# Kernel optimization log

Measured on AMD Instinct MI355X. Metric: run time of the kernel, lower is better.

The kernel has to match this reference:

```python
import jax, jax.numpy as jnp
import numpy as np
from math import factorial

# ---- architecture constants (from S2ConvNet_original.__init__) ----
B_IN, B_L1, B_L2 = 30, 15, 10
F1, F2, NCLS = 20, 40, 10
BATCH = 32

# ---------- numpy precompute: Wigner small-d matrices and quadrature ----------

def wigner_d(l, beta):
    """Wigner small-d matrix d^l_{m,n}(beta) for all m,n, vectorized over beta.
    Returns [len(beta), 2l+1, 2l+1] with centered indices (row m+l, col n+l)."""
    beta = np.atleast_1d(np.asarray(beta, dtype=np.float64))
    cb, sb = np.cos(beta / 2), np.sin(beta / 2)
    d = np.zeros((beta.size, 2 * l + 1, 2 * l + 1))
    for m in range(-l, l + 1):
        for n in range(-l, l + 1):
            pref = np.sqrt(float(factorial(l + m) * factorial(l - m) * factorial(l + n) * factorial(l - n)))
            s = np.zeros_like(beta)
            for k in range(max(0, m - n), min(l + m, l - n) + 1):
                c = (-1.0) ** k / float(factorial(k) * factorial(l + m - k) * factorial(l - n - k) * factorial(n - m + k))
                s += c * cb ** (2 * l + m - n - 2 * k) * sb ** (n - m + 2 * k)
            d[:, m + l, n + l] = pref * s
    return d

def wigner_stack(nl, betas):
    """Zero-padded stack of d^l matrices: [nl, n_beta, 2nl-1, 2nl-1], centered at nl-1."""
    M, c = 2 * nl - 1, nl - 1
    D = np.zeros((nl, len(betas), M, M))
    for l in range(nl):
        D[l, :, c - l:c + l + 1, c - l:c + l + 1] = wigner_d(l, betas)
    return D

def dh_weights(b):
    """Driscoll-Healy / SOFT quadrature weights over the 2b beta samples."""
    j = np.arange(2 * b); k = np.arange(b)
    s = (np.sin(np.outer(2 * j + 1, 2 * k + 1) * np.pi / (4 * b)) / (2 * k + 1)).sum(axis=1)
    return (2.0 / b) * np.sin(np.pi * (2 * j + 1) / (4 * b)) * s

def soft_betas(b):
    return np.pi * (2 * np.arange(2 * b) + 1) / (4 * b)

def centered_freqs(nl, n):
    # map centered m in [-(nl-1), nl-1] to fft bin indices of length-n transform
    return (np.arange(2 * nl - 1) - (nl - 1)) % n

# ---- conv1 (S2 -> SO3), b_in=30, b_out=15 ----
NL1, M1 = B_L1, 2 * B_L1 - 1
_D1F = wigner_stack(NL1, soft_betas(B_IN))[:, :, :, NL1 - 1] * dh_weights(B_IN)[None, :, None]  # [15,60,29]
_D1I = wigner_stack(NL1, soft_betas(B_L1))  # [15,30,29,29]
FQI1 = centered_freqs(NL1, 2 * B_IN)
FQO1 = centered_freqs(NL1, 2 * B_L1)
# s2_near_identity_grid: max_beta=pi/8, n_alpha=8, n_beta=3 -> 24 points
_gb = np.arange(1, 4) * (np.pi / 8) / 3
_ga = np.linspace(0, 2 * np.pi, 8, endpoint=False)
GB1, GA1 = [g.ravel() for g in np.meshgrid(_gb, _ga, indexing='ij')]
_m1 = np.arange(M1) - (NL1 - 1)
_Y1 = ((2 * np.arange(NL1) + 1.0)[:, None, None]
       * wigner_stack(NL1, GB1)[:, :, :, NL1 - 1].transpose(0, 2, 1)
       * np.exp(-1j * np.outer(_m1, GA1))[None])  # [15,29,24] spherical-harmonic basis at grid

# ---- conv2 (SO3 -> SO3), b_in=15, b_out=10 ----
NL2, M2 = B_L2, 2 * B_L2 - 1
_D2F = wigner_stack(NL2, soft_betas(B_L1)) * dh_weights(B_L1)[None, :, None, None]  # [10,30,19,19]
_D2I = wigner_stack(NL2, soft_betas(B_L2))  # [10,20,19,19]
FQI2 = centered_freqs(NL2, 2 * B_L1)
FQO2 = centered_freqs(NL2, 2 * B_L2)
# so3_near_identity_grid: 3 betas x 8 alphas x 8 gammas = 192 points
_gg = np.linspace(0, 2 * np.pi, 8, endpoint=False)
GB2, GA2, GG2 = [g.ravel() for g in np.meshgrid(_gb, _ga, _gg, indexing='ij')]
_m2 = np.arange(M2) - (NL2 - 1)
_Y2 = ((2 * np.arange(NL2) + 1.0)[:, None, None, None]
       * wigner_stack(NL2, GB2).transpose(0, 2, 3, 1)
       * np.exp(-1j * (np.outer(_m2, GA2)[:, None, :] + np.outer(_m2, GG2)[None, :, :]))[None])  # [10,19,19,192]

D1F = jnp.asarray(_D1F, jnp.float32); D1I = jnp.asarray(_D1I, jnp.float32); Y1 = jnp.asarray(_Y1, jnp.complex64)
D2F = jnp.asarray(_D2F, jnp.float32); D2I = jnp.asarray(_D2I, jnp.float32); Y2 = jnp.asarray(_Y2, jnp.complex64)
W_INT = jnp.asarray(dh_weights(B_L2), jnp.float32)  # [20]


def s2_conv(x, w, bias):
    # x: [B,1,60,60] (beta, alpha) -> SO3 signal [B,F1,30,30,30]
    xf = jnp.fft.fft(x, axis=-1)[..., FQI1]                       # [B,1,60,29] alpha-FFT, centered m
    X = jnp.einsum('bfjm,ljm->bflm', xf, D1F)                      # S2 FT: [B,1,15,29]
    psi = jnp.einsum('iog,lmg->lmio', w, Y1)                       # kernel S2 FT: [15,29,1,20]
    Z = jnp.einsum('bilm,lnio->bolmn', X, jnp.conj(psi))           # outer product m x n: [B,20,15,29,29]
    Fb = jnp.einsum('bolmn,ljmn->bojmn', Z, D1I)                   # beta synthesis: [B,20,30,29,29]
    n = 2 * B_L1
    full = jnp.zeros(Fb.shape[:3] + (n, n), Fb.dtype).at[..., FQO1[:, None], FQO1[None, :]].set(Fb)
    y = jnp.fft.ifft2(full, axes=(-2, -1)).real * (n * n)          # inverse alpha/gamma FFT
    return y + bias


def so3_conv(x, w, bias):
    # x: [B,F1,30,30,30] (beta, alpha, gamma) -> [B,F2,20,20,20]
    xf = jnp.fft.fft2(x, axes=(-2, -1))[..., FQI2[:, None], FQI2[None, :]]  # [B,20,30,19,19]
    X = jnp.einsum('bfjmn,ljmn->bflmn', xf, D2F)                   # SO3 FT: [B,20,10,19,19]
    psi = jnp.einsum('iog,lmng->lmnio', w, Y2)                     # kernel SO3 FT: [10,19,19,20,40]
    Z = jnp.einsum('bilmn,lknio->bolmk', X, jnp.conj(psi))         # Z^l = X^l @ Psi^l^H: [B,40,10,19,19]
    Fb = jnp.einsum('bolmk,ljmk->bojmk', Z, D2I)                   # [B,40,20,19,19]
    n = 2 * B_L2
    full = jnp.zeros(Fb.shape[:3] + (n, n), Fb.dtype).at[..., FQO2[:, None], FQO2[None, :]].set(Fb)
    y = jnp.fft.ifft2(full, axes=(-2, -1)).real * (n * n)
    return y + bias


def setup_inputs() -> dict:
    key = jax.random.key(0)
    ks = jax.random.split(key, 6)
    x = jax.random.normal(ks[0], (BATCH, 1, 2 * B_IN, 2 * B_IN), jnp.float32)
    w1 = jax.random.normal(ks[1], (1, F1, GB1.size), jnp.float32) / np.sqrt(GB1.size)
    b1 = jax.random.normal(ks[2], (1, F1, 1, 1, 1), jnp.float32) * 0.01
    w2 = jax.random.normal(ks[3], (F1, F2, GB2.size), jnp.float32) / np.sqrt(F1 * GB2.size)
    b2 = jax.random.normal(ks[4], (1, F2, 1, 1, 1), jnp.float32) * 0.01
    w_lin = jax.random.normal(ks[5], (NCLS, F2), jnp.float32) / np.sqrt(F2)
    bl_lin = jnp.zeros((NCLS,), jnp.float32)
    return {"x": x, "w1": w1, "b1": b1, "w2": w2, "b2": b2, "w_lin": w_lin, "bl_lin": bl_lin}


def reference(x, w1, b1, w2, b2, w_lin, bl_lin):
    h = jax.nn.relu(s2_conv(x, w1, b1))                            # [B,20,30,30,30]
    h = jax.nn.relu(so3_conv(h, w2, b2))                           # [B,40,20,20,20]
    # so3_integrate: quadrature over beta, uniform sums over alpha/gamma
    g = jnp.einsum('bfjkl,j->bf', h, W_INT) * (2 * np.pi / (2 * B_L2)) ** 2
    return g @ w_lin.T + bl_lin                                    # [B,10]
```

## Files before the change

kernel.cpp:

```cpp
#include <hip/hip_runtime.h>
#include <cmath>
#include <cstdio>

#ifndef M_PI
#define M_PI 3.14159265358979323846
#endif

#define OFF_D1F   0
#define OFF_D1IP  26100
#define OFF_D2FP  227940
#define OFF_D2IP  282090
#define OFF_Y1    318190
#define OFF_WI    339070
#define OFF_E1    339090
#define OFF_I1    342570
#define OFF_E2    344310
#define OFF_I2    345450
#define OFF_DHW30 346210
#define OFF_DHW15 346270
#define NCONST    346300

#define WOFF_CONST 0ul
#define WOFF_Y2BF  2457600ul
#define WOFF_W2BF  5406720ul
#define WOFF_AAUG  5750784ul
#define WOFF_BT    15581184ul
#define WOFF_H1    39174144ul
#define WOFF_CPSI  39174144ul
#define WOFF_Z     39174144ul
#define WOFF_H2    2457600ul
#define WOFF_XF1   76140544ul
#define WOFF_X1    (76140544ul + 445440ul)
#define WOFF_PSI1  (76140544ul + 445440ul + 111360ul)
#define WOFF_G     (76140544ul + 445440ul + 111360ul + 69600ul)
#define WS_NEED    (WOFF_G + 5120ul)

typedef __attribute__((ext_vector_type(8))) short short8v;
typedef __attribute__((ext_vector_type(4))) float f32x4;

__device__ inline unsigned short f2bf(float x){
  unsigned int u = __float_as_uint(x);
  u += 0x7FFFu + ((u >> 16) & 1u);
  return (unsigned short)(u >> 16);
}
__device__ inline float bf2f(unsigned short u){
  return __uint_as_float(((unsigned int)u) << 16);
}
__device__ inline unsigned int packbf(float a, float b){
  return (unsigned int)f2bf(a) | (((unsigned int)f2bf(b))<<16);
}

__device__ inline double dfact(int n){ double r=1.0; for(int i=2;i<=n;i++) r*=(double)i; return r; }
__device__ inline double dpowi(double x,int e){ double r=1.0; for(int i=0;i<e;i++) r*=x; return r; }
__device__ double wig(int l,int m,int n,double beta){
  if(m < -l || m > l || n < -l || n > l) return 0.0;
  double cb=cos(0.5*beta), sb=sin(0.5*beta);
  double pref=sqrt(dfact(l+m)*dfact(l-m)*dfact(l+n)*dfact(l-n));
  int k0 = (m-n)>0 ? (m-n) : 0;
  int k1 = (l+m) < (l-n) ? (l+m) : (l-n);
  double c0 = ((k0&1)?-1.0:1.0)/(dfact(k0)*dfact(l+m-k0)*dfact(l-n-k0)*dfact(n-m+k0));
  double t = c0 * dpowi(cb, 2*l+m-n-2*k0) * dpowi(sb, n-m+2*k0);
  double ratio = (sb*sb)/(cb*cb);
  double s = t;
  for(int k=k0;k<k1;k++){
    t *= -((double)(l+m-k)*(double)(l-n-k)) / ((double)(k+1)*(double)(n-m+k+1)) * ratio;
    s += t;
  }
  return pref*s;
}
__device__ inline double dh_w(int b,int j){
  double s=0.0;
  for(int k=0;k<b;k++) s += sin((2.0*j+1.0)*(2.0*k+1.0)*M_PI/(4.0*b))/(2.0*k+1.0);
  return (2.0/b)*sin(M_PI*(2.0*j+1.0)/(4.0*b))*s;
}
__device__ inline double soft_beta(int b,int j){ return M_PI*(2.0*j+1.0)/(4.0*b); }
__device__ inline void octcs(int q, double* c, double* s){
  const double r = 0.70710678118654752440;
  int i = q & 7;
  const double C[8]={1.0,r,0.0,-r,-1.0,-r,0.0,r};
  const double S[8]={0.0,r,1.0,r,0.0,-r,-1.0,-r};
  *c=C[i]; *s=S[i];
}

__global__ __launch_bounds__(256) void kconst0(float* __restrict__ C){
  for(int idx = blockIdx.x*256 + threadIdx.x; idx < 3670; idx += gridDim.x*256){
    if(idx < 20){ C[OFF_WI+idx]=(float)dh_w(10,idx); }
    else if(idx < 80){ int j=idx-20; C[OFF_DHW30+j]=(float)dh_w(30,j); }
    else if(idx < 110){ int j=idx-80; C[OFF_DHW15+j]=(float)dh_w(15,j); }
    else if(idx < 1850){ int q=idx-110;
      int a=q%60; int m=q/60; double ph=-2.0*M_PI*(double)(m-14)*a/60.0;
      C[OFF_E1+2*q]=(float)cos(ph); C[OFF_E1+2*q+1]=(float)sin(ph);
    } else if(idx < 2720){ int q=idx-1850;
      int m=q%29; int p=q/29; double ph=2.0*M_PI*(double)p*(double)(m-14)/30.0;
      C[OFF_I1+2*q]=(float)cos(ph); C[OFF_I1+2*q+1]=(float)sin(ph);
    } else if(idx < 3290){ int q=idx-2720;
      int a=q%30; int m=q/30; double ph=-2.0*M_PI*(double)(m-9)*a/30.0;
      C[OFF_E2+2*q]=(float)cos(ph); C[OFF_E2+2*q+1]=(float)sin(ph);
    } else { int q=idx-3290;
      int m=q%19; int p=q/19; double ph=2.0*M_PI*(double)p*(double)(m-9)/20.0;
      C[OFF_I2+2*q]=(float)cos(ph); C[OFF_I2+2*q+1]=(float)sin(ph);
    }
  }
}

__global__ __launch_bounds__(256) void kconst(float* __restrict__ C,
                                              unsigned int* __restrict__ Y2p){
  unsigned int* Cu = (unsigned int*)C;
  for(long idx = (long)blockIdx.x*blockDim.x + threadIdx.x; idx < 1065910L;
      idx += (long)gridDim.x*blockDim.x){
    if(idx < 26100L){
      int m=(int)(idx%29); int j=(int)((idx/29)%60); int l=(int)(idx/(29*60));
      C[OFF_D1F+idx] = (float)( wig(l, m-14, 0, soft_beta(30,j)) * (double)C[OFF_DHW30+j] );
    } else if(idx < 227940L){ long q=idx-26100L;
      int id=(int)(q%841); int lp=(int)((q/841)%8); int j=(int)(q/6728);
      int n=id/29, m=id%29;
      double beta=soft_beta(15,j);
      double w0=wig(2*lp,   m-14, n-14, beta);
      double w1=(2*lp+1<15)? wig(2*lp+1, m-14, n-14, beta) : 0.0;
      Cu[OFF_D1IP+q]=packbf((float)w0,(float)w1);
    } else if(idx < 282090L){ long q=idx-227940L;
      int id=(int)(q%361); int lp=(int)((q/361)%5); int j=(int)(q/1805);
      int m=id/19, n=id%19;
      double beta=soft_beta(15,j); double dw=(double)C[OFF_DHW15+j];
      double w0=wig(2*lp,   m-9, n-9, beta)*dw;
      double w1=wig(2*lp+1, m-9, n-9, beta)*dw;
      Cu[OFF_D2FP+q]=packbf((float)w0,(float)w1);
    } else if(idx < 318190L){ long q=idx-282090L;
      int id=(int)(q%361); int lp=(int)((q/361)%5); int j=(int)(q/1805);
      int m=id/19, n=id%19;
      double beta=soft_beta(10,j);
      double w0=wig(2*lp,   m-9, n-9, beta);
      double w1=wig(2*lp+1, m-9, n-9, beta);
      Cu[OFF_D2IP+q]=packbf((float)w0,(float)w1);
    } else if(idx < 328630L){ long q=idx-318190L;
      int g=(int)(q%24); int m=(int)((q/24)%29); int l=(int)(q/(24*29));
      double gb=((g>>3)+1)*(M_PI/8.0)/3.0;
      int ka = g&7;
      double mag=(2*l+1)*wig(l, m-14, 0, gb);
      double cc,ss; octcs((m-14)*ka, &cc, &ss);
      C[OFF_Y1+2*q]  =(float)(mag*cc);
      C[OFF_Y1+2*q+1]=(float)(-mag*ss);
    } else { long q=idx-328630L;
      int g2=(int)(q%96); int row=(int)((q/96)%768); int l=(int)(q/(96*768));
      unsigned int outv=0u;
      if(row<722){
        int kn=row>>1, ri=row&1, kk=kn/19, n=kn%19;
        int g0=2*g2;
        double gb=((g0>>6)+1)*(M_PI/8.0)/3.0;
        double mag=(2*l+1)*wig(l,kk-9,n-9,gb);
        int ka=(g0>>3)&7;
        double c0,s0,c1,s1;
        octcs((kk-9)*ka + (n-9)*(g0&7), &c0,&s0);
        octcs((kk-9)*ka + (n-9)*((g0+1)&7), &c1,&s1);
        float v0 = ri ? (float)(-mag*s0) : (float)(mag*c0);
        float v1 = ri ? (float)(-mag*s1) : (float)(mag*c1);
        outv = (unsigned int)f2bf(v0) | (((unsigned int)f2bf(v1))<<16);
      }
      Y2p[q]=outv;
    }
  }
}

__global__ __launch_bounds__(256) void kfill(uint4* __restrict__ p, long n16){
  uint4 z; z.x=0u; z.y=0u; z.z=0u; z.w=0u;
  for(long i=(long)blockIdx.x*256+threadIdx.x; i<n16; i+=(long)gridDim.x*256) p[i]=z;
}

__global__ __launch_bounds__(256) void kw2(const float* __restrict__ w2,
                                           unsigned int* __restrict__ w2bf){
  int idx = blockIdx.x*256 + threadIdx.x;
  if(idx >= 896*96) return;
  int row=idx/96, g2=idx%96;
  float a=0.f, b=0.f;
  if(row<800){ a=w2[row*192+2*g2]; b=w2[row*192+2*g2+1]; }
  w2bf[idx] = (unsigned int)f2bf(a) | (((unsigned int)f2bf(b))<<16);
}


__global__ __launch_bounds__(256) void k1a(const float* __restrict__ x,
                                           const float2* __restrict__ E1,
                                           float2* __restrict__ xf1){
  int idx = blockIdx.x*256 + threadIdx.x;
  if(idx >= 32*60*29) return;
  int m = idx % 29; int bj = idx / 29;
  const float* row = x + bj*60;
  float sr=0.f, si=0.f;
  for(int a=0;a<60;a++){ float2 e=E1[m*60+a]; float v=row[a]; sr+=v*e.x; si+=v*e.y; }
  xf1[idx] = make_float2(sr,si);
}

__global__ __launch_bounds__(256) void k1b(const float2* __restrict__ xf1,
                                           const float* __restrict__ D1F,
                                           float2* __restrict__ X1){
  int idx = blockIdx.x*256 + threadIdx.x;
  if(idx >= 32*15*29) return;
  int m = idx % 29; int lb = idx / 29; int l = lb % 15; int b = lb / 15;
  float sr=0.f, si=0.f;
  for(int j=0;j<60;j++){
    float d = D1F[(l*60+j)*29+m]; float2 v = xf1[(b*60+j)*29+m];
    sr += d*v.x; si += d*v.y;
  }
  X1[(b*15+l)*29+m] = make_float2(sr,si);
}

__global__ __launch_bounds__(256) void kpsi1(const float* __restrict__ w1,
                                             const float2* __restrict__ Y1,
                                             float2* __restrict__ psi1cO){
  int idx = blockIdx.x*256 + threadIdx.x;
  if(idx >= 15*29*20) return;
  int o = idx % 20; int ln = idx / 20;
  float sr=0.f, si=0.f;
  for(int g=0;g<24;g++){ float w=w1[o*24+g]; float2 y=Y1[ln*24+g]; sr+=w*y.x; si+=w*y.y; }
  psi1cO[o*435 + ln] = make_float2(sr,-si);
}

#define JC 6
__global__ __launch_bounds__(512) void k2(const float2* __restrict__ X1,
                                          const float2* __restrict__ psi1cO,
                                          const unsigned int* __restrict__ D1IP,
                                          const float2* __restrict__ I1g,
                                          const float* __restrict__ b1,
                                          unsigned short* __restrict__ h1){
  int o=blockIdx.x, b=blockIdx.y, j0=blockIdx.z*JC;
  __shared__ float2 sX[15][29];
  __shared__ float2 sP[15][29];
  __shared__ __align__(16) unsigned short I1A[64][72];
  __shared__ __align__(16) unsigned short I1C[32][72];
  __shared__ __align__(16) unsigned short U[JC*32*72];
  int t=threadIdx.x;
  for(int q=t;q<435;q+=512){ ((float2*)sX)[q]=X1[b*435+q]; ((float2*)sP)[q]=psi1cO[o*435+q]; }
  for(int q=t;q<64*72;q+=512){
    int R=q/72, k=q%72; float v=0.f;
    if(k<64){ int kk=k&31, kh=k>>5;
      if(kk<29){
        if(R<30){ float2 e=I1g[R*29+kk]; v = kh ? -e.y : e.x; }
        else if(R>=32 && R<62){ float2 e=I1g[(R-32)*29+kk]; v = kh ? e.x : e.y; }
      }
    }
    I1A[R][k]=f2bf(v);
  }
  for(int q=t;q<32*72;q+=512){
    int Qr=q/72, k=q%72; float v=0.f;
    if(Qr<30 && k<64){ int kk=k&31, kh=k>>5;
      if(kk<29){ float2 e=I1g[Qr*29+kk]; v = kh ? -e.y : e.x; }
    }
    I1C[Qr][k]=f2bf(v);
  }
  for(int q=t;q<JC*32*36;q+=512) ((unsigned int*)U)[q]=0u;
  __syncthreads();
  float Pr[2][16], Pi[2][16];
  #pragma unroll
  for(int s=0;s<2;s++){
    int id=t+512*s;
    if(id<841){
      int n=id/29, m=id%29;
      #pragma unroll
      for(int l=0;l<15;l++){
        float2 xx=sX[l][m], pp=sP[l][n];
        Pr[s][l]=xx.x*pp.x-xx.y*pp.y;
        Pi[s][l]=xx.x*pp.y+xx.y*pp.x;
      }
      Pr[s][15]=0.f; Pi[s][15]=0.f;
    }
  }
  int wid=t>>6, lane=t&63;
  int fr=lane&15, fc=lane&15, rq=(lane>>4)*4, ko=(lane>>4)*8;
  float bias=b1[o];
  #pragma unroll
  for(int s=0;s<2;s++){
    int id=t+512*s;
    if(id<841){
      int n=id/29, m=id%29;
      for(int jr=0;jr<JC;jr++){
        const unsigned int* dp = D1IP + (size_t)(j0+jr)*6728 + id;
        float ar=0.f, ai=0.f;
        #pragma unroll
        for(int p=0;p<8;p++){
          unsigned int v = dp[p*841];
          float f0=__uint_as_float(v<<16);
          float f1=__uint_as_float(v&0xFFFF0000u);
          ar += Pr[s][2*p]*f0 + Pr[s][2*p+1]*f1;
          ai += Pi[s][2*p]*f0 + Pi[s][2*p+1]*f1;
        }
        U[(jr*32+n)*72 + m]    = f2bf(ar);
        U[(jr*32+n)*72 + 32+m] = f2bf(ai);
      }
    }
  }
  __syncthreads();
  f32x4 accB[JC];
  #pragma unroll
  for(int u=0;u<JC;u++){
    int tile = wid + 8*u;
    int mt = tile/(2*JC), nt = tile%(2*JC);
    short8v a0=*(const short8v*)&I1A[16*mt+fr][ko];
    short8v a1=*(const short8v*)&I1A[16*mt+fr][32+ko];
    short8v b0=*(const short8v*)&U[(16*nt+fr)*72+ko];
    short8v b1=*(const short8v*)&U[(16*nt+fr)*72+32+ko];
    f32x4 ac={0.f,0.f,0.f,0.f};
    ac=__builtin_amdgcn_mfma_f32_16x16x32_bf16(a0,b0,ac,0,0,0);
    ac=__builtin_amdgcn_mfma_f32_16x16x32_bf16(a1,b1,ac,0,0,0);
    accB[u]=ac;
  }
  __syncthreads();
  #pragma unroll
  for(int u=0;u<JC;u++){
    int tile = wid + 8*u;
    int mt = tile/(2*JC), nt = tile%(2*JC);
    #pragma unroll
    for(int r=0;r<4;r++){
      int R=16*mt+rq+r;
      int jn=16*nt+fc;
      int p=R&31, hi=R>>5, jj=jn>>5, n=jn&31;
      U[p*(JC*64) + jj*64 + hi*32 + n] = f2bf(accB[u][r]);
    }
  }
  __syncthreads();
  #pragma unroll
  for(int u=0;u<(4*JC+7)/8;u++){
    int tile = wid + 8*u;
    if(tile < 4*JC){
      int jj=tile>>2, sub=tile&3, mtC=sub>>1, ntC=sub&1;
      short8v a0=*(const short8v*)&U[(16*mtC+fr)*(JC*64) + jj*64 + ko];
      short8v a1=*(const short8v*)&U[(16*mtC+fr)*(JC*64) + jj*64 + 32 + ko];
      short8v b0=*(const short8v*)&I1C[16*ntC+fr][ko];
      short8v b1=*(const short8v*)&I1C[16*ntC+fr][32+ko];
      f32x4 ac={0.f,0.f,0.f,0.f};
      ac=__builtin_amdgcn_mfma_f32_16x16x32_bf16(a0,b0,ac,0,0,0);
      ac=__builtin_amdgcn_mfma_f32_16x16x32_bf16(a1,b1,ac,0,0,0);
      size_t base=((size_t)(b*20+o)*30+(j0+jj))*900;
      #pragma unroll
      for(int r=0;r<4;r++){
        int p=16*mtC+rq+r, qq=16*ntC+fc;
        if(p<30 && qq<30){
          float v=fmaxf(ac[r]+bias,0.f);
          h1[base+p*30+qq]=f2bf(v);
        }
      }
    }
  }
}

__global__ __launch_bounds__(256) void k3g(const unsigned short* __restrict__ A,
                                           const unsigned short* __restrict__ B,
                                           float* __restrict__ Cf){
  int l = blockIdx.z;
  int m0 = blockIdx.y*128, n0 = blockIdx.x*128;
  __shared__ unsigned short As[128][40];
  __shared__ unsigned short Bs[128][40];
  int t = threadIdx.x;
  int wid = t>>6, lane = t&63;
  int wr = wid>>1, wc = wid&1;
  f32x4 acc[4][4];
  #pragma unroll
  for(int a=0;a<4;a++)
    #pragma unroll
    for(int c=0;c<4;c++) acc[a][c]=(f32x4){0.f,0.f,0.f,0.f};
  const unsigned short* Ag = A;
  const unsigned short* Bg = B + (size_t)l*768*192;
  int row_a = wr*64 + (lane&15);
  int row_b = wc*64 + (lane&15);
  int ko = (lane>>4)*8;
  for(int kt=0; kt<192; kt+=32){
    #pragma unroll
    for(int it=0; it<2; it++){
      int q = t + 256*it;
      int r = q>>2, c8 = (q&3)*8;
      *(uint4*)&As[r][c8] = *(const uint4*)&Ag[(size_t)(m0+r)*192 + kt + c8];
      *(uint4*)&Bs[r][c8] = *(const uint4*)&Bg[(size_t)(n0+r)*192 + kt + c8];
    }
    __syncthreads();
    short8v af[4], bfv[4];
    #pragma unroll
    for(int f=0; f<4; f++){
      af[f]  = *(const short8v*)&As[row_a + f*16][ko];
      bfv[f] = *(const short8v*)&Bs[row_b + f*16][ko];
    }
    #pragma unroll
    for(int fm=0;fm<4;fm++)
      #pragma unroll
      for(int fn=0;fn<4;fn++)
        acc[fm][fn] = __builtin_amdgcn_mfma_f32_16x16x32_bf16(af[fm], bfv[fn], acc[fm][fn], 0,0,0);
    __syncthreads();
  }
  #pragma unroll
  for(int fm=0;fm<4;fm++){
    int mb = m0 + wr*64 + fm*16 + ((lane>>4)*4);
    #pragma unroll
    for(int fn=0;fn<4;fn++){
      int n = n0 + wc*64 + fn*16 + (lane&15);
      #pragma unroll
      for(int r=0;r<4;r++){
        Cf[((size_t)(l*896)+mb+r)*768 + n] = acc[fm][fn][r];
      }
    }
  }
}

__global__ __launch_bounds__(384) void kBt(const float* __restrict__ Cf,
                                           unsigned short* __restrict__ Bt){
  int c = blockIdx.x;
  int l = blockIdx.y;
  int t = threadIdx.x;
  if(t>=380) return;
  int i=t/19, n=t%19;
  int o=c/19, kk=c%19;
  float2 v = *(const float2*)&Cf[((size_t)(l*896) + i*40+o)*768 + (kk*19+n)*2];
  float zr = v.x, zi = -v.y;
  unsigned short* base = Bt + (size_t)l*1536*768;
  size_t r0=(size_t)(2*c)*768, r1=r0+768;
  int col=i*19+n;
  base[r0+col]     = f2bf(zr);
  base[r0+384+col] = f2bf(-zi);
  base[r1+col]     = f2bf(zi);
  base[r1+384+col] = f2bf(zr);
}

__global__ __launch_bounds__(512) void k4(const unsigned short* __restrict__ h1,
                                          const unsigned int* __restrict__ D2FP,
                                          const float2* __restrict__ E2g,
                                          unsigned short* __restrict__ Aaug){
  int i=blockIdx.x, b=blockIdx.y;
  __shared__ __align__(16) unsigned short E2c[48][32];
  __shared__ __align__(16) unsigned short E2A[48][64];
  __shared__ __align__(16) unsigned short T1[192][72];
  __shared__ __align__(16) unsigned short U2[192][44];
  int t=threadIdx.x;
  for(int q=t;q<48*32;q+=512){
    int R=q>>5, g=q&31; float v=0.f;
    if(R<38 && g<30){ float2 e=E2g[(R%19)*30+g]; v=(R<19)? e.x : e.y; }
    E2c[R][g]=f2bf(v);
  }
  for(int q=t;q<48*64;q+=512){
    int R=q>>6, c=q&63; float v=0.f;
    if(R<38){
      int mm=R%19; int mi=(R>=19);
      if(c<30){ float2 e=E2g[mm*30+c]; v = mi ? e.y : e.x; }
      else if(c>=32 && c<62){ float2 e=E2g[mm*30+(c-32)]; v = mi ? e.x : -e.y; }
    }
    E2A[R][c]=f2bf(v);
  }
  for(int q=t;q<192*72;q+=512) T1[q/72][q%72]=0;
  for(int q=t;q<192*44;q+=512) U2[q/44][q%44]=0;
  float accr[10], acci[10];
  #pragma unroll
  for(int l=0;l<10;l++){ accr[l]=0.f; acci[l]=0.f; }
  int m3=t/19, n3=t%19;
  int wid=t>>6, lane=t&63, fr=lane&15, fc=lane&15, ko=(lane>>4)*8, rq=(lane>>4)*4;
  size_t blk=(size_t)(b*20+i)*27000;
  const unsigned int* h1u=(const unsigned int*)h1;
  __syncthreads();
  for(int p=0;p<3;p++){
    int j0=p*10;
    for(int mt=wid; mt<19; mt+=8){
      int rg=16*mt+fr;
      size_t base=blk + (size_t)j0*900 + (size_t)rg*30 + ko;
      union{ unsigned int u[4]; short8v v; } A;
      const unsigned int* pp=h1u + (base>>1);
      A.u[0]=pp[0]; A.u[1]=pp[1]; A.u[2]=pp[2]; A.u[3]=pp[3];
      #pragma unroll
      for(int nt=0;nt<3;nt++){
        short8v Bf=*(const short8v*)&E2c[16*nt+fr][ko];
        f32x4 ac={0.f,0.f,0.f,0.f};
        ac=__builtin_amdgcn_mfma_f32_16x16x32_bf16(A.v,Bf,ac,0,0,0);
        int np=16*nt+fc;
        if(np<38){
          int ri=(np>=19), nn=np-19*ri;
          #pragma unroll
          for(int r=0;r<4;r++){
            int rgw=16*mt+rq+r;
            if(rgw<300){
              int jr=rgw/30, a=rgw%30;
              T1[jr*19+nn][32*ri+a]=f2bf(ac[r]);
            }
          }
        }
      }
    }
    __syncthreads();
    for(int u=0;u<5;u++){
      int tile=wid+8*u; if(tile>=36) break;
      int mt2=tile/12, nt2=tile%12;
      short8v a0=*(const short8v*)&E2A[16*mt2+fr][ko];
      short8v a1=*(const short8v*)&E2A[16*mt2+fr][32+ko];
      short8v b0=*(const short8v*)&T1[16*nt2+fr][ko];
      short8v b1=*(const short8v*)&T1[16*nt2+fr][32+ko];
      f32x4 ac={0.f,0.f,0.f,0.f};
      ac=__builtin_amdgcn_mfma_f32_16x16x32_bf16(a0,b0,ac,0,0,0);
      ac=__builtin_amdgcn_mfma_f32_16x16x32_bf16(a1,b1,ac,0,0,0);
      int jn=16*nt2+fc;
      if(jn<190){
        #pragma unroll
        for(int r=0;r<4;r++){
          int R=16*mt2+rq+r;
          if(R<38) U2[jn][R]=f2bf(ac[r]);
        }
      }
    }
    __syncthreads();
    if(t<361){
      for(int jr=0;jr<10;jr++){
        int jg=j0+jr;
        const unsigned int* dp = D2FP + (size_t)jg*1805 + t;
        float xr=bf2f(U2[jr*19+n3][m3]);
        float xi=bf2f(U2[jr*19+n3][19+m3]);
        #pragma unroll
        for(int pp2=0;pp2<5;pp2++){
          unsigned int v=dp[pp2*361];
          float f0=__uint_as_float(v<<16);
          float f1=__uint_as_float(v&0xFFFF0000u);
          accr[2*pp2]  +=f0*xr; acci[2*pp2]  +=f0*xi;
          accr[2*pp2+1]+=f1*xr; acci[2*pp2+1]+=f1*xi;
        }
      }
    }
  }
  if(t<361){
    #pragma unroll
    for(int l=0;l<10;l++){
      size_t row=((size_t)(l*640) + b*19+m3)*768;
      Aaug[row + i*19+n3]       = f2bf(accr[l]);
      Aaug[row + 384 + i*19+n3] = f2bf(acci[l]);
    }
  }
}

__global__ __launch_bounds__(256) void k5(const unsigned short* __restrict__ A,
                                          const unsigned short* __restrict__ B,
                                          float* __restrict__ Cf){
  int l = blockIdx.z;
  int m0 = blockIdx.y*128, n0 = blockIdx.x*128;
  __shared__ unsigned short As[128][40];
  __shared__ unsigned short Bs[128][40];
  int t = threadIdx.x;
  int wid = t>>6, lane = t&63;
  int wr = wid>>1, wc = wid&1;
  f32x4 acc[4][4];
  #pragma unroll
  for(int a=0;a<4;a++)
    #pragma unroll
    for(int c=0;c<4;c++) acc[a][c]=(f32x4){0.f,0.f,0.f,0.f};
  const unsigned short* Ag = A + (size_t)l*640*768;
  const unsigned short* Bg = B + (size_t)l*1536*768;
  int row_a = wr*64 + (lane&15);
  int row_b = wc*64 + (lane&15);
  int ko = (lane>>4)*8;
  for(int kt=0; kt<768; kt+=32){
    #pragma unroll
    for(int it=0; it<2; it++){
      int q = t + 256*it;
      int r = q>>2, c8 = (q&3)*8;
      *(uint4*)&As[r][c8] = *(const uint4*)&Ag[(size_t)(m0+r)*768 + kt + c8];
      *(uint4*)&Bs[r][c8] = *(const uint4*)&Bg[(size_t)(n0+r)*768 + kt + c8];
    }
    __syncthreads();
    short8v af[4], bfv[4];
    #pragma unroll
    for(int f=0; f<4; f++){
      af[f]  = *(const short8v*)&As[row_a + f*16][ko];
      bfv[f] = *(const short8v*)&Bs[row_b + f*16][ko];
    }
    #pragma unroll
    for(int fm=0;fm<4;fm++)
      #pragma unroll
      for(int fn=0;fn<4;fn++)
        acc[fm][fn] = __builtin_amdgcn_mfma_f32_16x16x32_bf16(af[fm], bfv[fn], acc[fm][fn], 0,0,0);
    __syncthreads();
  }
  #pragma unroll
  for(int fm=0;fm<4;fm++){
    int mb = m0 + wr*64 + fm*16 + ((lane>>4)*4);
    #pragma unroll
    for(int fn=0;fn<4;fn++){
      int n = n0 + wc*64 + fn*16 + (lane&15);
      if(n<1520){
        #pragma unroll
        for(int r=0;r<4;r++){
          int m = mb + r;
          if(m<608) Cf[((size_t)(l*608)+m)*1520 + n] = acc[fm][fn][r];
        }
      }
    }
  }
}

__global__ __launch_bounds__(512) void k6(const float2* __restrict__ Z,
                                          const unsigned int* __restrict__ D2IP,
                                          const float2* __restrict__ I2g,
                                          const float* __restrict__ b2,
                                          unsigned short* __restrict__ h2){
  int o=blockIdx.x, b=blockIdx.y;
  __shared__ __align__(16) unsigned short U[29952];
  __shared__ __align__(16) unsigned short I2A[48][72];
  __shared__ __align__(16) unsigned short I2C[32][72];
  int t=threadIdx.x;
  for(int q=t;q<14976;q+=512) ((unsigned int*)U)[q]=0u;
  for(int q=t;q<48*72;q+=512){
    int R=q/72, kd=q%72; float v=0.f;
    if(kd<38){
      int mm = (kd<19)? kd : kd-19; int hi = (kd>=19);
      if(R<20){ float2 e=I2g[R*19+mm]; v = hi ? -e.y : e.x; }
      else if(R<40){ float2 e=I2g[(R-20)*19+mm]; v = hi ? e.x : e.y; }
    }
    I2A[R][kd]=f2bf(v);
  }
  for(int q=t;q<32*72;q+=512){
    int Qr=q/72, kd=q%72; float v=0.f;
    if(Qr<20 && kd<38){
      int kk2 = (kd<19)? kd : kd-19; int hi = (kd>=19);
      float2 e=I2g[Qr*19+kk2]; v = hi ? -e.y : e.x;
    }
    I2C[Qr][kd]=f2bf(v);
  }
  float zr[10], zi[10];
  int m=t/19, kk=t%19;
  if(t<361){
    #pragma unroll
    for(int l=0;l<10;l++){
      float2 z=Z[(size_t)(l*608 + b*19+m)*760 + o*19+kk];
      zr[l]=z.x; zi[l]=z.y;
    }
  }
  __syncthreads();
  if(t<361){
    for(int j=0;j<20;j++){
      const unsigned int* dp = D2IP + (size_t)j*1805 + t;
      float ar=0.f, ai=0.f;
      #pragma unroll
      for(int p=0;p<5;p++){
        unsigned int v=dp[p*361];
        float f0=__uint_as_float(v<<16);
        float f1=__uint_as_float(v&0xFFFF0000u);
        ar += zr[2*p]*f0 + zr[2*p+1]*f1;
        ai += zi[2*p]*f0 + zi[2*p+1]*f1;
      }
      U[(j*19+kk)*72 + m]      = f2bf(ar);
      U[(j*19+kk)*72 + 19 + m] = f2bf(ai);
    }
  }
  __syncthreads();
  int wid=t>>6, lane=t&63, fr=lane&15, ko=(lane>>4)*8;
  f32x4 acc1[9];
  #pragma unroll
  for(int u=0;u<9;u++){
    int tile=wid+8*u;
    int mt=tile/24, nt=tile%24;
    short8v a0=*(const short8v*)&I2A[16*mt+fr][ko];
    short8v a1=*(const short8v*)&I2A[16*mt+fr][32+ko];
    short8v bb0=*(const short8v*)&U[(16*nt+fr)*72+ko];
    short8v bb1=*(const short8v*)&U[(16*nt+fr)*72+32+ko];
    f32x4 ac={0.f,0.f,0.f,0.f};
    ac=__builtin_amdgcn_mfma_f32_16x16x32_bf16(a0,bb0,ac,0,0,0);
    ac=__builtin_amdgcn_mfma_f32_16x16x32_bf16(a1,bb1,ac,0,0,0);
    acc1[u]=ac;
  }
  __syncthreads();
  #pragma unroll
  for(int u=0;u<9;u++){
    int tile=wid+8*u; int mt=tile/24, nt=tile%24;
    #pragma unroll
    for(int r=0;r<4;r++){
      int R=16*mt+(lane>>4)*4+r;
      int n=16*nt+fr;
      if(R<40 && n<380){
        int j=n/19, kq=n%19;
        U[(j*20 + (R%20))*72 + (R/20)*19 + kq] = f2bf(acc1[u][r]);
      }
    }
  }
  __syncthreads();
  float bias=b2[o];
  size_t obase=((size_t)b*40+o)*8000;
  #pragma unroll
  for(int u=0;u<7;u++){
    int tile=wid+8*u;
    if(tile<52){
      int mt=tile>>1, nt=tile&1;
      short8v a0=*(const short8v*)&U[(16*mt+fr)*72+ko];
      short8v a1=*(const short8v*)&U[(16*mt+fr)*72+32+ko];
      short8v bb0=*(const short8v*)&I2C[16*nt+fr][ko];
      short8v bb1=*(const short8v*)&I2C[16*nt+fr][32+ko];
      f32x4 ac={0.f,0.f,0.f,0.f};
      ac=__builtin_amdgcn_mfma_f32_16x16x32_bf16(a0,bb0,ac,0,0,0);
      ac=__builtin_amdgcn_mfma_f32_16x16x32_bf16(a1,bb1,ac,0,0,0);
      #pragma unroll
      for(int r=0;r<4;r++){
        int row=16*mt+(lane>>4)*4+r;
        int q=16*nt+fr;
        if(row<400 && q<20){
          float v=fmaxf(ac[r]+bias,0.f);
          h2[obase + row*20 + q]=f2bf(v);
        }
      }
    }
  }
}

__global__ __launch_bounds__(256) void k7a(const unsigned int* __restrict__ h2p,
                                           const float* __restrict__ WI,
                                           float* __restrict__ g){
  int bf=blockIdx.x;
  const unsigned int* base=h2p + (size_t)bf*4000;
  int t=threadIdx.x; float s=0.f;
  for(int q=t;q<4000;q+=256){
    unsigned int v=base[q];
    float w=WI[q/200];
    s += (bf2f((unsigned short)(v&0xFFFF))+bf2f((unsigned short)(v>>16)))*w;
  }
  __shared__ float red[256];
  red[t]=s; __syncthreads();
  for(int off=128;off>0;off>>=1){ if(t<off) red[t]+=red[t+off]; __syncthreads(); }
  if(t==0){
    const float c=(float)((2.0*M_PI/20.0)*(2.0*M_PI/20.0));
    g[bf]=red[0]*c;
  }
}

__global__ __launch_bounds__(64) void k7b(const float* __restrict__ g,
                                          const float* __restrict__ wlin,
                                          const float* __restrict__ bl,
                                          float* __restrict__ out){
  int idx=blockIdx.x*64+threadIdx.x;
  if(idx>=320) return;
  int b=idx/10, c=idx%10;
  float s=bl[c];
  for(int f=0;f<40;f++) s += g[b*40+f]*wlin[c*40+f];
  out[b*10+c]=s;
}

extern "C" void kernel_launch(void* const* d_in, const int* in_sizes, int n_in,
                              void* d_out, int out_size, void* d_ws, size_t ws_size,
                              hipStream_t stream){
  (void)in_sizes; (void)n_in; (void)out_size;
  const float* x    = (const float*)d_in[0];
  const float* w1   = (const float*)d_in[1];
  const float* b1   = (const float*)d_in[2];
  const float* w2   = (const float*)d_in[3];
  const float* b2   = (const float*)d_in[4];
  const float* wlin = (const float*)d_in[5];
  const float* bl   = (const float*)d_in[6];
  float* out = (float*)d_out;
  char*  ws  = (char*)d_ws;

  if(ws_size < WS_NEED){
    fprintf(stderr, "kernel_launch: ws too small: have %zu need %lu\n", ws_size, WS_NEED);
  }

  float* C = (float*)(ws + WOFF_CONST);
  const float*  D1F = C + OFF_D1F;
  const unsigned int* D1IP = (const unsigned int*)C + OFF_D1IP;
  const unsigned int* D2FP = (const unsigned int*)C + OFF_D2FP;
  const unsigned int* D2IP = (const unsigned int*)C + OFF_D2IP;
  const float2* Y1  = (const float2*)(C + OFF_Y1);
  const float*  WI  = C + OFF_WI;
  const float2* E1  = (const float2*)(C + OFF_E1);
  const float2* I1  = (const float2*)(C + OFF_I1);
  const float2* E2  = (const float2*)(C + OFF_E2);
  const float2* I2  = (const float2*)(C + OFF_I2);

  float2* xf1   = (float2*)(ws + WOFF_XF1);
  float2* X1    = (float2*)(ws + WOFF_X1);
  float2* psi1c = (float2*)(ws + WOFF_PSI1);
  unsigned short* h1   = (unsigned short*)(ws + WOFF_H1);
  unsigned short* Y2bf = (unsigned short*)(ws + WOFF_Y2BF);
  unsigned short* w2bf = (unsigned short*)(ws + WOFF_W2BF);
  float*  Cpsi  = (float*)(ws + WOFF_CPSI);
  unsigned short* Aaug = (unsigned short*)(ws + WOFF_AAUG);
  unsigned short* Bt   = (unsigned short*)(ws + WOFF_BT);
  float*  Zf    = (float*)(ws + WOFF_Z);
  unsigned short* h2 = (unsigned short*)(ws + WOFF_H2);
  float*  g     = (float*)(ws + WOFF_G);

  hipLaunchKernelGGL(kconst0, dim3(16), dim3(256), 0, stream, C);
  hipLaunchKernelGGL(kconst, dim3(2048), dim3(256), 0, stream, C, (unsigned int*)Y2bf);
  hipLaunchKernelGGL(kfill, dim3(2048), dim3(256), 0, stream,
                     (uint4*)(ws + WOFF_AAUG), (long)(33423360ul/16ul));
  hipLaunchKernelGGL(kfill, dim3(1), dim3(256), 0, stream,
                     (uint4*)(ws + WOFF_H1 + 34560000ul), 32L);
  hipLaunchKernelGGL(kw2, dim3((896*96+255)/256), dim3(256), 0, stream, w2, (unsigned int*)w2bf);

  hipLaunchKernelGGL(k1a, dim3((32*60*29+255)/256), dim3(256), 0, stream, x, E1, xf1);
  hipLaunchKernelGGL(k1b, dim3((32*15*29+255)/256), dim3(256), 0, stream, xf1, D1F, X1);
  hipLaunchKernelGGL(kpsi1, dim3((15*29*20+255)/256), dim3(256), 0, stream, w1, Y1, psi1c);
  hipLaunchKernelGGL(k2, dim3(20,32,5), dim3(512), 0, stream, X1, psi1c, D1IP, I1, b1, h1);
  hipLaunchKernelGGL(k4, dim3(20,32), dim3(512), 0, stream, h1, D2FP, E2, Aaug);
  hipLaunchKernelGGL(k3g, dim3(6,7,10), dim3(256), 0, stream, w2bf, Y2bf, Cpsi);
  hipLaunchKernelGGL(kBt, dim3(760,10), dim3(384), 0, stream, Cpsi, Bt);
  hipLaunchKernelGGL(k5, dim3(12,5,10), dim3(256), 0, stream, Aaug, Bt, Zf);
  hipLaunchKernelGGL(k6, dim3(40,32), dim3(512), 0, stream, (const float2*)Zf, D2IP, I2, b2, h2);
  hipLaunchKernelGGL(k7a, dim3(1280), dim3(256), 0, stream, (const unsigned int*)h2, WI, g);
  hipLaunchKernelGGL(k7b, dim3(5), dim3(64), 0, stream, g, wlin, bl, out);
}
```

Before: 421.6 us.

## Widen k2 to 896 threads so each thread handles one output element

Raises k2's block size from 512 to 896 threads, so the 841 (n,m) work items map one per thread instead of two passes per thread. The 14 waves now split the MFMA tiles with stride 14, and the transposed U layout uses a padded row stride (TLS=392) to cut LDS bank conflicts. The inner accumulation uses split accumulators to shorten dependency chains. In exchange, the larger block may limit occupancy through register pressure under the 896-thread launch bound, and some waves sit idle in the MFMA stages.

```diff
diff --git a/kernel.cpp b/kernel.cpp
--- a/kernel.cpp
+++ b/kernel.cpp
@@ -215,7 +215,8 @@
 }
 
 #define JC 6
-__global__ __launch_bounds__(512) void k2(const float2* __restrict__ X1,
+#define TLS 392
+__global__ __launch_bounds__(896) void k2(const float2* __restrict__ X1,
                                           const float2* __restrict__ psi1cO,
                                           const unsigned int* __restrict__ D1IP,
                                           const float2* __restrict__ I1g,
@@ -228,8 +229,8 @@
   __shared__ __align__(16) unsigned short I1C[32][72];
   __shared__ __align__(16) unsigned short U[JC*32*72];
   int t=threadIdx.x;
-  for(int q=t;q<435;q+=512){ ((float2*)sX)[q]=X1[b*435+q]; ((float2*)sP)[q]=psi1cO[o*435+q]; }
-  for(int q=t;q<64*72;q+=512){
+  for(int q=t;q<435;q+=896){ ((float2*)sX)[q]=X1[b*435+q]; ((float2*)sP)[q]=psi1cO[o*435+q]; }
+  for(int q=t;q<64*72;q+=896){
     int R=q/72, k=q%72; float v=0.f;
     if(k<64){ int kk=k&31, kh=k>>5;
       if(kk<29){
@@ -239,90 +240,91 @@
     }
     I1A[R][k]=f2bf(v);
   }
-  for(int q=t;q<32*72;q+=512){
+  for(int q=t;q<32*72;q+=896){
     int Qr=q/72, k=q%72; float v=0.f;
     if(Qr<30 && k<64){ int kk=k&31, kh=k>>5;
       if(kk<29){ float2 e=I1g[Qr*29+kk]; v = kh ? -e.y : e.x; }
     }
     I1C[Qr][k]=f2bf(v);
   }
-  for(int q=t;q<JC*32*36;q+=512) ((unsigned int*)U)[q]=0u;
-  __syncthreads();
-  float Pr[2][16], Pi[2][16];
-  #pragma unroll
-  for(int s=0;s<2;s++){
-    int id=t+512*s;
-    if(id<841){
-      int n=id/29, m=id%29;
-      #pragma unroll
-      for(int l=0;l<15;l++){
-        float2 xx=sX[l][m], pp=sP[l][n];
-        Pr[s][l]=xx.x*pp.x-xx.y*pp.y;
-        Pi[s][l]=xx.x*pp.y+xx.y*pp.x;
-      }
-      Pr[s][15]=0.f; Pi[s][15]=0.f;
+  for(int q=t;q<JC*32*36;q+=896) ((unsigned int*)U)[q]=0u;
+  __syncthreads();
+  float2 PrP[8], PiP[8];
+  int idn=t/29, idm=t%29;
+  if(t<841){
+    #pragma unroll
+    for(int p=0;p<8;p++){
+      int l0=2*p, l1=2*p+1;
+      float2 xx0=sX[l0][idm], pp0=sP[l0][idn];
+      PrP[p].x = xx0.x*pp0.x - xx0.y*pp0.y;
+      PiP[p].x = xx0.x*pp0.y + xx0.y*pp0.x;
+      if(l1<15){
+        float2 xx1=sX[l1][idm], pp1=sP[l1][idn];
+        PrP[p].y = xx1.x*pp1.x - xx1.y*pp1.y;
+        PiP[p].y = xx1.x*pp1.y + xx1.y*pp1.x;
+      } else { PrP[p].y=0.f; PiP[p].y=0.f; }
     }
   }
   int wid=t>>6, lane=t&63;
   int fr=lane&15, fc=lane&15, rq=(lane>>4)*4, ko=(lane>>4)*8;
   float bias=b1[o];
-  #pragma unroll
-  for(int s=0;s<2;s++){
-    int id=t+512*s;
-    if(id<841){
-      int n=id/29, m=id%29;
-      for(int jr=0;jr<JC;jr++){
-        const unsigned int* dp = D1IP + (size_t)(j0+jr)*6728 + id;
-        float ar=0.f, ai=0.f;
-        #pragma unroll
-        for(int p=0;p<8;p++){
-          unsigned int v = dp[p*841];
-          float f0=__uint_as_float(v<<16);
-          float f1=__uint_as_float(v&0xFFFF0000u);
-          ar += Pr[s][2*p]*f0 + Pr[s][2*p+1]*f1;
-          ai += Pi[s][2*p]*f0 + Pi[s][2*p+1]*f1;
-        }
-        U[(jr*32+n)*72 + m]    = f2bf(ar);
-        U[(jr*32+n)*72 + 32+m] = f2bf(ai);
-      }
-    }
-  }
-  __syncthreads();
-  f32x4 accB[JC];
-  #pragma unroll
-  for(int u=0;u<JC;u++){
-    int tile = wid + 8*u;
-    int mt = tile/(2*JC), nt = tile%(2*JC);
-    short8v a0=*(const short8v*)&I1A[16*mt+fr][ko];
-    short8v a1=*(const short8v*)&I1A[16*mt+fr][32+ko];
-    short8v b0=*(const short8v*)&U[(16*nt+fr)*72+ko];
-    short8v b1=*(const short8v*)&U[(16*nt+fr)*72+32+ko];
-    f32x4 ac={0.f,0.f,0.f,0.f};
-    ac=__builtin_amdgcn_mfma_f32_16x16x32_bf16(a0,b0,ac,0,0,0);
-    ac=__builtin_amdgcn_mfma_f32_16x16x32_bf16(a1,b1,ac,0,0,0);
-    accB[u]=ac;
-  }
-  __syncthreads();
-  #pragma unroll
-  for(int u=0;u<JC;u++){
-    int tile = wid + 8*u;
-    int mt = tile/(2*JC), nt = tile%(2*JC);
-    #pragma unroll
-    for(int r=0;r<4;r++){
-      int R=16*mt+rq+r;
-      int jn=16*nt+fc;
-      int p=R&31, hi=R>>5, jj=jn>>5, n=jn&31;
-      U[p*(JC*64) + jj*64 + hi*32 + n] = f2bf(accB[u][r]);
-    }
-  }
-  __syncthreads();
-  #pragma unroll
-  for(int u=0;u<(4*JC+7)/8;u++){
-    int tile = wid + 8*u;
+  if(t<841){
+    for(int jr=0;jr<JC;jr++){
+      const unsigned int* dp = D1IP + (size_t)(j0+jr)*6728 + t;
+      float arx=0.f, ary=0.f, aix=0.f, aiy=0.f;
+      #pragma unroll
+      for(int p=0;p<8;p++){
+        unsigned int v = dp[p*841];
+        float f0=__uint_as_float(v<<16);
+        float f1=__uint_as_float(v&0xFFFF0000u);
+        arx += PrP[p].x*f0; ary += PrP[p].y*f1;
+        aix += PiP[p].x*f0; aiy += PiP[p].y*f1;
+      }
+      U[(jr*32+idn)*72 + idm]    = f2bf(arx+ary);
+      U[(jr*32+idn)*72 + 32+idm] = f2bf(aix+aiy);
+    }
+  }
+  __syncthreads();
+  f32x4 accB[4];
+  #pragma unroll
+  for(int u=0;u<4;u++){
+    int tile = wid + 14*u;
+    accB[u]=(f32x4){0.f,0.f,0.f,0.f};
+    if(tile < 4*2*JC){
+      int mt = tile/(2*JC), nt = tile%(2*JC);
+      short8v a0=*(const short8v*)&I1A[16*mt+fr][ko];
+      short8v a1=*(const short8v*)&I1A[16*mt+fr][32+ko];
+      short8v b0=*(const short8v*)&U[(16*nt+fr)*72+ko];
+      short8v b1=*(const short8v*)&U[(16*nt+fr)*72+32+ko];
+      f32x4 ac={0.f,0.f,0.f,0.f};
+      ac=__builtin_amdgcn_mfma_f32_16x16x32_bf16(a0,b0,ac,0,0,0);
+      ac=__builtin_amdgcn_mfma_f32_16x16x32_bf16(a1,b1,ac,0,0,0);
+      accB[u]=ac;
+    }
+  }
+  __syncthreads();
+  #pragma unroll
+  for(int u=0;u<4;u++){
+    int tile = wid + 14*u;
+    if(tile < 4*2*JC){
+      int mt = tile/(2*JC), nt = tile%(2*JC);
+      #pragma unroll
+      for(int r=0;r<4;r++){
+        int R=16*mt+rq+r;
+        int jn=16*nt+fc;
+        int p=R&31, hi=R>>5, jj=jn>>5, n=jn&31;
+        U[p*TLS + jj*64 + hi*32 + n] = f2bf(accB[u][r]);
+      }
+    }
+  }
+  __syncthreads();
+  #pragma unroll
+  for(int u=0;u<2;u++){
+    int tile = wid + 14*u;
     if(tile < 4*JC){
       int jj=tile>>2, sub=tile&3, mtC=sub>>1, ntC=sub&1;
-      short8v a0=*(const short8v*)&U[(16*mtC+fr)*(JC*64) + jj*64 + ko];
-      short8v a1=*(const short8v*)&U[(16*mtC+fr)*(JC*64) + jj*64 + 32 + ko];
+      short8v a0=*(const short8v*)&U[(16*mtC+fr)*TLS + jj*64 + ko];
+      short8v a1=*(const short8v*)&U[(16*mtC+fr)*TLS + jj*64 + 32 + ko];
       short8v b0=*(const short8v*)&I1C[16*ntC+fr][ko];
       short8v b1=*(const short8v*)&I1C[16*ntC+fr][32+ko];
       f32x4 ac={0.f,0.f,0.f,0.f};
@@ -782,7 +784,7 @@
   hipLaunchKernelGGL(k1a, dim3((32*60*29+255)/256), dim3(256), 0, stream, x, E1, xf1);
   hipLaunchKernelGGL(k1b, dim3((32*15*29+255)/256), dim3(256), 0, stream, xf1, D1F, X1);
   hipLaunchKernelGGL(kpsi1, dim3((15*29*20+255)/256), dim3(256), 0, stream, w1, Y1, psi1c);
-  hipLaunchKernelGGL(k2, dim3(20,32,5), dim3(512), 0, stream, X1, psi1c, D1IP, I1, b1, h1);
+  hipLaunchKernelGGL(k2, dim3(20,32,5), dim3(896), 0, stream, X1, psi1c, D1IP, I1, b1, h1);
   hipLaunchKernelGGL(k4, dim3(20,32), dim3(512), 0, stream, h1, D2FP, E2, Aaug);
   hipLaunchKernelGGL(k3g, dim3(6,7,10), dim3(256), 0, stream, w2bf, Y2bf, Cpsi);
   hipLaunchKernelGGL(kBt, dim3(760,10), dim3(384), 0, stream, Cpsi, Bt);
```

After: 452.0 us. 1.07x slower.
